# Kernel optimization log

Hardware: AMD Instinct MI355X
Metric: run time of the kernel (lower is better)

The kernel has to match this reference:

```python
import jax, jax.numpy as jnp
import numpy as np

N = 30000        # nodes
E = 600000       # edges
R = 32           # relations
NB = 30          # num_bases
D = 128          # entity_dim == hidden_dim == output_dim
H = 8            # heads, head dim C = D // H = 16
NUM_ENT = 100000
NGRAPH = 16      # graphs in batch
L = 2            # num_rgcn_layers == num_transformer_layers
EPS = 1e-5


def _ln(x, g, b):
    mu = x.mean(-1, keepdims=True)
    var = ((x - mu) ** 2).mean(-1, keepdims=True)
    return (x - mu) * jax.lax.rsqrt(var + EPS) * g + b


def setup_inputs() -> dict:
    key = jax.random.key(0)
    ks = iter(jax.random.split(key, 48))

    def nrm(shape, s=0.05):
        return jax.random.normal(next(ks), shape, jnp.float32) * s

    inp = {}
    inp["node_ids"] = jax.random.randint(next(ks), (N,), 0, NUM_ENT)
    inp["edge_index"] = jax.random.randint(next(ks), (2, E), 0, N)
    inp["edge_type"] = jax.random.randint(next(ks), (E,), 0, R)
    inp["batch"] = jnp.sort(jax.random.randint(next(ks), (N,), 0, NGRAPH))
    inp["entity_emb"] = nrm((NUM_ENT, D)).at[0].set(0.0)  # padding_idx=0
    inp["rel_emb"] = nrm((R, D)).at[0].set(0.0)           # padding_idx=0
    inp["rgcn_comp"] = nrm((L, R, NB))
    inp["rgcn_bases"] = nrm((L, NB, D, D))
    inp["rgcn_root"] = nrm((L, D, D))
    inp["rgcn_bias"] = jnp.zeros((L, D), jnp.float32)
    inp["rgcn_ln_g"] = jnp.ones((L, D), jnp.float32)
    inp["rgcn_ln_b"] = jnp.zeros((L, D), jnp.float32)
    inp["tr_wq"] = nrm((L, D, D)); inp["tr_bq"] = jnp.zeros((L, D), jnp.float32)
    inp["tr_wk"] = nrm((L, D, D)); inp["tr_bk"] = jnp.zeros((L, D), jnp.float32)
    inp["tr_wv"] = nrm((L, D, D)); inp["tr_bv"] = jnp.zeros((L, D), jnp.float32)
    inp["tr_we"] = nrm((L, D, D))                          # lin_edge (bias=False in PyG)
    inp["tr_wskip"] = nrm((L, D, D)); inp["tr_bskip"] = jnp.zeros((L, D), jnp.float32)
    inp["tr_ln_g"] = jnp.ones((L, D), jnp.float32)
    inp["tr_ln_b"] = jnp.zeros((L, D), jnp.float32)
    return inp


def reference(node_ids, edge_index, edge_type, batch, entity_emb, rel_emb,
              rgcn_comp, rgcn_bases, rgcn_root, rgcn_bias, rgcn_ln_g, rgcn_ln_b,
              tr_wq, tr_bq, tr_wk, tr_bk, tr_wv, tr_bv, tr_we, tr_wskip, tr_bskip,
              tr_ln_g, tr_ln_b):
    src, tgt = edge_index[0], edge_index[1]
    C = D // H
    x = entity_emb[node_ids]            # [N, D]
    edge_attr = rel_emb[edge_type]      # [E, D]

    # ---- RGCN layers: basis decomposition, mean aggregation per (target, relation) ----
    seg = tgt * R + edge_type
    cnt = jax.ops.segment_sum(jnp.ones((E,), jnp.float32), seg, num_segments=N * R)
    inv = jnp.where(cnt > 0, 1.0 / jnp.maximum(cnt, 1.0), 0.0)   # [N*R]
    for l in range(L):
        agg = jax.ops.segment_sum(x[src], seg, num_segments=N * R)   # [N*R, D]
        agg = (agg * inv[:, None]).reshape(N, R, D)
        w = jnp.einsum('rb,bio->rio', rgcn_comp[l], rgcn_bases[l])   # [R, D, D]
        x = jnp.einsum('nri,rio->no', agg, w) + x @ rgcn_root[l] + rgcn_bias[l]
        x = jax.nn.relu(_ln(x, rgcn_ln_g[l], rgcn_ln_b[l]))          # dropout = identity (eval)

    # ---- TransformerConv layers: edge-conditioned multi-head attention ----
    for l in range(L):
        q = (x @ tr_wq[l] + tr_bq[l]).reshape(N, H, C)
        k = (x @ tr_wk[l] + tr_bk[l]).reshape(N, H, C)
        v = (x @ tr_wv[l] + tr_bv[l]).reshape(N, H, C)
        e = (edge_attr @ tr_we[l]).reshape(E, H, C)
        kj = k[src] + e                                              # [E, H, C]
        vj = v[src] + e
        alpha = jnp.einsum('ehc,ehc->eh', q[tgt], kj) / np.float32(np.sqrt(C))
        m = jax.ops.segment_max(alpha, tgt, num_segments=N)          # [N, H]
        a = jnp.exp(alpha - m[tgt])
        denom = jax.ops.segment_sum(a, tgt, num_segments=N)
        a = a / jnp.maximum(denom[tgt], 1e-16)                       # softmax per target node
        out = jax.ops.segment_sum((vj * a[:, :, None]).reshape(E, D), tgt, num_segments=N)
        out = out + x @ tr_wskip[l] + tr_bskip[l]                    # root/skip connection
        out = jax.nn.relu(_ln(out, tr_ln_g[l], tr_ln_b[l]))          # dropout = identity (eval)
        x = x + out                                                  # dims match -> residual

    cnt_g = jax.ops.segment_sum(jnp.ones((N,), jnp.float32), batch, num_segments=NGRAPH)
    graph_emb = jax.ops.segment_sum(x, batch, num_segments=NGRAPH) / jnp.maximum(cnt_g, 1.0)[:, None]
    return x, graph_emb
```

## Files before the change

kernel.cpp:

```cpp
#include <hip/hip_runtime.h>

#define NN 30000
#define NE 600000
#define RR 32
#define NBASE 30
#define NG 16

typedef long long i64;
typedef unsigned short ushort;
typedef short bf16x8 __attribute__((ext_vector_type(8)));
typedef float f32x4 __attribute__((ext_vector_type(4)));

__device__ __forceinline__ ushort f2bf(float f){
  unsigned u = __float_as_uint(f);
  u += 0x7fffu + ((u >> 16) & 1u);
  return (ushort)(u >> 16);
}
__device__ __forceinline__ float bf2f(ushort u){
  return __uint_as_float(((unsigned)u) << 16);
}
__device__ __forceinline__ unsigned pk2(float a, float b){
  return (unsigned)f2bf(a) | ((unsigned)f2bf(b) << 16);
}

__global__ void k_gather(const float* __restrict__ emb, const int* __restrict__ ids,
                         float* __restrict__ x, ushort* __restrict__ xb){
  int t = blockIdx.x*256 + threadIdx.x;
  if (t >= NN*32) return;
  int n = t >> 5, c = t & 31;
  float4 v = ((const float4*)emb)[(i64)ids[n]*32 + c];
  ((float4*)x)[(i64)n*32 + c] = v;
  *(uint2*)&xb[(i64)n*128 + c*4] = make_uint2(pk2(v.x, v.y), pk2(v.z, v.w));
}

__global__ void k_cnt(const int* __restrict__ tgt, const int* __restrict__ ety,
                      float* __restrict__ cnt){
  int e = blockIdx.x*256 + threadIdx.x;
  if (e >= NE) return;
  atomicAdd(&cnt[(i64)tgt[e]*RR + ety[e]], 1.0f);
}

__global__ void k_hist_blk(const int* __restrict__ ety, int* __restrict__ hist){
  __shared__ int lh[RR];
  if (threadIdx.x < RR) lh[threadIdx.x] = 0;
  __syncthreads();
  int e0 = blockIdx.x*2048 + threadIdx.x;
  #pragma unroll
  for (int i = 0; i < 8; i++){
    int e = e0 + i*256;
    if (e < NE) atomicAdd(&lh[ety[e]], 1);
  }
  __syncthreads();
  if (threadIdx.x < RR){
    int v = lh[threadIdx.x];
    if (v) atomicAdd(&hist[threadIdx.x], v);
  }
}

__global__ void k_scan(const int* __restrict__ hist, int* __restrict__ base,
                       int* __restrict__ cursor, int* __restrict__ pb,
                       int* __restrict__ pb64){
  if (threadIdx.x != 0 || blockIdx.x != 0) return;
  int s = 0, p = 0, p64 = 0;
  for (int r = 0; r < RR; r++){
    base[r] = s; cursor[r] = s; pb[r] = p; pb64[r] = p64;
    s += hist[r]; p += (hist[r] + 127) >> 7; p64 += (hist[r] + 63) >> 6;
  }
  base[RR] = s; pb[RR] = p; pb64[RR] = p64;
}

__global__ __launch_bounds__(256) void k_scatter_blk(const int* __restrict__ ety,
    int* __restrict__ cursor, int* __restrict__ eord){
  __shared__ int lh[RR];
  __shared__ int lb[RR];
  if (threadIdx.x < RR) lh[threadIdx.x] = 0;
  __syncthreads();
  int e0 = blockIdx.x*2048 + threadIdx.x;
  #pragma unroll
  for (int i = 0; i < 8; i++){
    int e = e0 + i*256;
    if (e < NE) atomicAdd(&lh[ety[e]], 1);
  }
  __syncthreads();
  if (threadIdx.x < RR){
    int c = lh[threadIdx.x];
    lb[threadIdx.x] = c ? atomicAdd(&cursor[threadIdx.x], c) : 0;
  }
  __syncthreads();
  if (threadIdx.x < RR) lh[threadIdx.x] = 0;
  __syncthreads();
  #pragma unroll
  for (int i = 0; i < 8; i++){
    int e = e0 + i*256;
    if (e < NE){
      int r = ety[e];
      int loc = atomicAdd(&lh[r], 1);
      eord[lb[r] + loc] = e;
    }
  }
}

__global__ void k_hist2(const int* __restrict__ etgt, int* __restrict__ hist2){
  int e = blockIdx.x*256 + threadIdx.x;
  if (e >= NE) return;
  atomicAdd(&hist2[etgt[e]], 1);
}

__global__ __launch_bounds__(1024) void k_scan2(const int* __restrict__ hist2,
    int* __restrict__ rowptr, int* __restrict__ cursor2){
  __shared__ int s[1024];
  int t = threadIdx.x;
  int base = t*30;
  int loc[30];
  int sum = 0;
  #pragma unroll
  for (int i = 0; i < 30; i++){
    int v = (base+i < NN) ? hist2[base+i] : 0;
    loc[i] = sum; sum += v;
  }
  s[t] = sum; __syncthreads();
  for (int off = 1; off < 1024; off <<= 1){
    int v = (t >= off) ? s[t-off] : 0;
    __syncthreads();
    s[t] += v;
    __syncthreads();
  }
  int excl = (t > 0) ? s[t-1] : 0;
  #pragma unroll
  for (int i = 0; i < 30; i++){
    int idx = base + i;
    if (idx <= NN){
      rowptr[idx] = excl + loc[i];
      if (idx < NN) cursor2[idx] = excl + loc[i];
    }
  }
}

__global__ void k_scatter2(const int* __restrict__ etgt, const int* __restrict__ esrc,
                           const int* __restrict__ ety, int* __restrict__ cursor2,
                           int2* __restrict__ se2, int* __restrict__ pos2){
  int e = blockIdx.x*256 + threadIdx.x;
  if (e >= NE) return;
  int q = atomicAdd(&cursor2[etgt[e]], 1);
  se2[q] = make_int2(esrc[e], ety[e]);
  pos2[e] = q;
}

__global__ void k_basis(const float* __restrict__ comp, const float* __restrict__ bases,
                        float* __restrict__ wT, ushort* __restrict__ wTb){
  int t = blockIdx.x*256 + threadIdx.x;
  int r = t >> 14, rem = t & 16383, c = rem >> 7, kk = rem & 127;
  float acc = 0.f;
  for (int b = 0; b < NBASE; b++)
    acc += comp[r*NBASE + b] * bases[(i64)b*16384 + kk*128 + c];
  wT[t] = acc;
  wTb[t] = f2bf(acc);
}

__global__ void k_tw(const float* __restrict__ root, const float* __restrict__ wq,
                     const float* __restrict__ wk, const float* __restrict__ wv,
                     const float* __restrict__ wsk, ushort* __restrict__ out){
  int z = blockIdx.y;
  const float* srcs[5] = {root, wq, wk, wv, wsk};
  const float* S = srcs[z >> 1] + (i64)(z & 1)*16384;
  int idx = blockIdx.x*256 + threadIdx.x;
  int c = idx >> 7, kk = idx & 127;
  out[(i64)z*16384 + idx] = f2bf(S[kk*128 + c]);
}


__global__ __launch_bounds__(256, 2) void k_mm_mfma(const ushort* __restrict__ xb,
    const ushort* __restrict__ wTb, const float* __restrict__ bias,
    float* __restrict__ Y, int nrows){
  __shared__ ushort Xs[16384];
  __shared__ ushort Ws[16384];
  int t = threadIdx.x;
  int row0 = blockIdx.x * 128;
  for (int i = t; i < 2048; i += 256){
    int row = i >> 4, c = i & 15;
    *(uint4*)((char*)Ws + row*256 + ((c*16) ^ ((row&7)<<4))) =
        *(const uint4*)((const char*)wTb + row*256 + c*16);
    int gr = min(row0 + row, nrows - 1);
    *(uint4*)((char*)Xs + row*256 + ((c*16) ^ ((row&7)<<4))) =
        *(const uint4*)((const char*)(xb + (i64)gr*128) + c*16);
  }
  __syncthreads();
  int w = t >> 6, l = t & 63;
  int wm = w >> 1, wn = w & 1;
  int lrow = l & 15, lg = l >> 4;
  int swz = (lrow & 7) << 4;
  const char* pX = (const char*)Xs + (wm*64 + lrow)*256;
  const char* pW = (const char*)Ws + (wn*64 + lrow)*256;
  f32x4 acc[4][4] = {};
  #pragma unroll
  for (int ks = 0; ks < 4; ks++){
    int kb = (16*lg + 64*ks) ^ swz;
    bf16x8 a[4], bx[4];
    #pragma unroll
    for (int ns = 0; ns < 4; ns++) a[ns]  = *(const bf16x8*)(pW + ns*4096 + kb);
    #pragma unroll
    for (int ms = 0; ms < 4; ms++) bx[ms] = *(const bf16x8*)(pX + ms*4096 + kb);
    #pragma unroll
    for (int ms = 0; ms < 4; ms++)
      #pragma unroll
      for (int ns = 0; ns < 4; ns++)
        acc[ms][ns] = __builtin_amdgcn_mfma_f32_16x16x32_bf16(a[ns], bx[ms], acc[ms][ns], 0, 0, 0);
  }
  #pragma unroll
  for (int ms = 0; ms < 4; ms++){
    int m = row0 + wm*64 + ms*16 + lrow;
    if (m >= nrows) continue;
    #pragma unroll
    for (int ns = 0; ns < 4; ns++){
      int n0 = wn*64 + ns*16 + 4*lg;
      float4 bv = *(const float4*)&bias[n0];
      f32x4 v = acc[ms][ns];
      *(float4*)&Y[(i64)m*128 + n0] =
          make_float4(v[0]+bv.x, v[1]+bv.y, v[2]+bv.z, v[3]+bv.w);
    }
  }
}

__global__ __launch_bounds__(256, 2) void k_mm4(const ushort* __restrict__ xb,
    const ushort* __restrict__ wTb, int layer,
    const float* __restrict__ biq, const float* __restrict__ bik,
    const float* __restrict__ biv, const float* __restrict__ bisk,
    ushort* __restrict__ qo, ushort* __restrict__ ko, ushort* __restrict__ vo,
    float* __restrict__ z, int nrows){
  __shared__ ushort Xs[16384];
  __shared__ ushort Ws[16384];
  int t = threadIdx.x;
  int row0 = blockIdx.x * 128;
  for (int i = t; i < 2048; i += 256){
    int row = i >> 4, c = i & 15;
    int gr = min(row0 + row, nrows - 1);
    *(uint4*)((char*)Xs + row*256 + ((c*16) ^ ((row&7)<<4))) =
        *(const uint4*)((const char*)(xb + (i64)gr*128) + c*16);
  }
  int w = t >> 6, l = t & 63;
  int wm = w >> 1, wn = w & 1;
  int lrow = l & 15, lg = l >> 4;
  int swz = (lrow & 7) << 4;
  const char* pX = (const char*)Xs + (wm*64 + lrow)*256;
  const char* pW = (const char*)Ws + (wn*64 + lrow)*256;
  const float* biases[4] = {biq, bik, biv, bisk};
  ushort* outs[3] = {qo, ko, vo};
  #pragma unroll 1
  for (int arr = 0; arr < 4; arr++){
    const ushort* Wg = wTb + (i64)(2 + 2*arr + layer)*16384;
    __syncthreads();
    for (int i = t; i < 2048; i += 256){
      int row = i >> 4, c = i & 15;
      *(uint4*)((char*)Ws + row*256 + ((c*16) ^ ((row&7)<<4))) =
          *(const uint4*)((const char*)Wg + row*256 + c*16);
    }
    __syncthreads();
    f32x4 acc[4][4] = {};
    #pragma unroll
    for (int ks = 0; ks < 4; ks++){
      int kb = (16*lg + 64*ks) ^ swz;
      bf16x8 a[4], bx[4];
      #pragma unroll
      for (int ns = 0; ns < 4; ns++) a[ns]  = *(const bf16x8*)(pW + ns*4096 + kb);
      #pragma unroll
      for (int ms = 0; ms < 4; ms++) bx[ms] = *(const bf16x8*)(pX + ms*4096 + kb);
      #pragma unroll
      for (int ms = 0; ms < 4; ms++)
        #pragma unroll
        for (int ns = 0; ns < 4; ns++)
          acc[ms][ns] = __builtin_amdgcn_mfma_f32_16x16x32_bf16(a[ns], bx[ms], acc[ms][ns], 0, 0, 0);
    }
    const float* bias = biases[arr];
    #pragma unroll
    for (int ms = 0; ms < 4; ms++){
      int m = row0 + wm*64 + ms*16 + lrow;
      if (m >= nrows) continue;
      #pragma unroll
      for (int ns = 0; ns < 4; ns++){
        int n0 = wn*64 + ns*16 + 4*lg;
        float4 bv = *(const float4*)&bias[n0];
        f32x4 v = acc[ms][ns];
        if (arr < 3){
          *(uint2*)&outs[arr][(i64)m*128 + n0] =
              make_uint2(pk2(v[0]+bv.x, v[1]+bv.y), pk2(v[2]+bv.z, v[3]+bv.w));
        } else {
          *(float4*)&z[(i64)m*128 + n0] =
              make_float4(v[0]+bv.x, v[1]+bv.y, v[2]+bv.z, v[3]+bv.w);
        }
      }
    }
  }
}

__global__ __launch_bounds__(256, 2) void k_edge_mfma(const int* __restrict__ esrc,
    const int* __restrict__ etgt, const int* __restrict__ eord,
    const int* __restrict__ pos2, const int* __restrict__ hist,
    const int* __restrict__ base, const int* __restrict__ pb,
    const float* __restrict__ cnt, const ushort* __restrict__ xb,
    const ushort* __restrict__ wb, ushort* __restrict__ y){
  __shared__ ushort Xs[16384];
  __shared__ ushort Ws[16384];
  __shared__ int s_src[128];
  __shared__ int s_p2[128];
  __shared__ float s_inv[128];
  int b = blockIdx.x;
  int r = -1;
  #pragma unroll 1
  for (int i = 0; i < RR; i++){
    if (b >= pb[i] && b < pb[i+1]) { r = i; break; }
  }
  if (r < 0) return;
  int chunk = b - pb[r];
  int rowbase = base[r] + chunk*128;
  int nvalid = min(128, hist[r] - chunk*128);
  int t = threadIdx.x;
  if (t < 128){
    bool valid = t < nvalid;
    int eid = eord[rowbase + (valid ? t : 0)];
    s_src[t] = esrc[eid];
    s_p2[t]  = valid ? pos2[eid] : NE;
    s_inv[t] = valid ? (1.0f / cnt[(i64)etgt[eid]*RR + r]) : 0.0f;
  }
  __syncthreads();
  const ushort* Wg = wb + (i64)r*16384;
  for (int i = t; i < 2048; i += 256){
    int row = i >> 4, c = i & 15;
    *(uint4*)((char*)Ws + row*256 + ((c*16) ^ ((row&7)<<4))) =
        *(const uint4*)((const char*)Wg + row*256 + c*16);
    *(uint4*)((char*)Xs + row*256 + ((c*16) ^ ((row&7)<<4))) =
        *(const uint4*)((const char*)(xb + (i64)s_src[row]*128) + c*16);
  }
  __syncthreads();
  int w = t >> 6, l = t & 63;
  int wm = w >> 1, wn = w & 1;
  int lrow = l & 15, lg = l >> 4;
  int swz = (lrow & 7) << 4;
  const char* pX = (const char*)Xs + (wm*64 + lrow)*256;
  const char* pW = (const char*)Ws + (wn*64 + lrow)*256;
  f32x4 acc[4][4] = {};
  #pragma unroll
  for (int ks = 0; ks < 4; ks++){
    int kb = (16*lg + 64*ks) ^ swz;
    bf16x8 a[4], bx[4];
    #pragma unroll
    for (int ns = 0; ns < 4; ns++) a[ns]  = *(const bf16x8*)(pW + ns*4096 + kb);
    #pragma unroll
    for (int ms = 0; ms < 4; ms++) bx[ms] = *(const bf16x8*)(pX + ms*4096 + kb);
    #pragma unroll
    for (int ms = 0; ms < 4; ms++)
      #pragma unroll
      for (int ns = 0; ns < 4; ns++)
        acc[ms][ns] = __builtin_amdgcn_mfma_f32_16x16x32_bf16(a[ns], bx[ms], acc[ms][ns], 0, 0, 0);
  }
  #pragma unroll
  for (int ms = 0; ms < 4; ms++){
    int m = wm*64 + ms*16 + lrow;
    float sc = s_inv[m];
    i64 yrow = (i64)s_p2[m] * 128;
    #pragma unroll
    for (int ns = 0; ns < 4; ns++){
      int n0 = wn*64 + ns*16 + 4*lg;
      f32x4 v = acc[ms][ns];
      *(uint2*)&y[yrow + n0] = make_uint2(pk2(v[0]*sc, v[1]*sc), pk2(v[2]*sc, v[3]*sc));
    }
  }
}

__global__ __launch_bounds__(256) void k_edge_atomic(const int* __restrict__ esrc,
    const int* __restrict__ etgt, const int* __restrict__ eord,
    const int* __restrict__ hist, const int* __restrict__ base,
    const int* __restrict__ pb, const float* __restrict__ cnt,
    const float* __restrict__ x, const float* __restrict__ wT,
    float* __restrict__ z){
  __shared__ float Xs[64][132];
  __shared__ int s_src[64];
  __shared__ int s_tgt[64];
  __shared__ float s_inv[64];
  int b = blockIdx.x;
  int r = -1;
  #pragma unroll 1
  for (int i = 0; i < RR; i++){
    if (b >= pb[i] && b < pb[i+1]) { r = i; break; }
  }
  if (r < 0) return;
  int chunk = b - pb[r];
  int rowbase = base[r] + chunk*64;
  int cnt_r = hist[r];
  if (threadIdx.x < 64){
    int i = threadIdx.x;
    bool valid = (chunk*64 + i) < cnt_r;
    int eid = valid ? eord[rowbase + i] : 0;
    int sv = valid ? esrc[eid] : 0;
    int tv = valid ? etgt[eid] : 0;
    s_src[i] = sv; s_tgt[i] = tv;
    s_inv[i] = valid ? (1.0f / cnt[(i64)tv*RR + r]) : 0.0f;
  }
  __syncthreads();
  for (int idx = threadIdx.x; idx < 64*32; idx += 256){
    int rr = idx >> 5, c4 = idx & 31;
    *(float4*)&Xs[rr][c4*4] = ((const float4*)x)[(i64)s_src[rr]*32 + c4];
  }
  __syncthreads();
  const float* W = wT + (i64)r*16384;
  int m = threadIdx.x & 15, cg = threadIdx.x >> 4;
  float acc[4][8] = {};
  #pragma unroll 2
  for (int k4 = 0; k4 < 128; k4 += 4){
    float4 xv[4], wv[8];
    #pragma unroll
    for (int i = 0; i < 4; i++) xv[i] = *(float4*)&Xs[m + 16*i][k4];
    #pragma unroll
    for (int j = 0; j < 8; j++) wv[j] = *(const float4*)&W[(i64)(cg + 16*j)*128 + k4];
    #pragma unroll
    for (int i = 0; i < 4; i++)
      #pragma unroll
      for (int j = 0; j < 8; j++)
        acc[i][j] += xv[i].x*wv[j].x + xv[i].y*wv[j].y + xv[i].z*wv[j].z + xv[i].w*wv[j].w;
  }
  #pragma unroll
  for (int i = 0; i < 4; i++){
    int rr = m + 16*i;
    float sc = s_inv[rr];
    i64 o = (i64)s_tgt[rr]*128;
    #pragma unroll
    for (int j = 0; j < 8; j++)
      atomicAdd(&z[o + cg + 16*j], acc[i][j]*sc);
  }
}

__global__ void k_seg(const int* __restrict__ rowptr, const ushort* __restrict__ y,
                      const float* __restrict__ z, const float* __restrict__ g,
                      const float* __restrict__ b, float* __restrict__ x,
                      ushort* __restrict__ xb){
  int t = (blockIdx.x*256 + threadIdx.x) >> 6;
  int l = threadIdx.x & 63;
  if (t >= NN) return;
  int q0 = rowptr[t], q1 = rowptr[t+1];
  float ax = 0.f, ay = 0.f;
  for (int q = q0; q < q1; q++){
    ushort2 u = *(const ushort2*)&y[(i64)q*128 + 2*l];
    ax += bf2f(u.x); ay += bf2f(u.y);
  }
  float2 zv = *(const float2*)&z[(i64)t*128 + 2*l];
  float tx = ax + zv.x, ty = ay + zv.y;
  float s = tx + ty;
  #pragma unroll
  for (int o = 1; o < 64; o <<= 1) s += __shfl_xor(s, o);
  float mu = s * 0.0078125f;
  float dx = tx - mu, dy = ty - mu;
  float s2 = dx*dx + dy*dy;
  #pragma unroll
  for (int o = 1; o < 64; o <<= 1) s2 += __shfl_xor(s2, o);
  float rs = rsqrtf(s2 * 0.0078125f + 1e-5f);
  float2 gg = *(const float2*)&g[2*l];
  float2 bb = *(const float2*)&b[2*l];
  float o0 = fmaxf(dx*rs*gg.x + bb.x, 0.f);
  float o1 = fmaxf(dy*rs*gg.y + bb.y, 0.f);
  *(float2*)&x[(i64)t*128 + 2*l] = make_float2(o0, o1);
  xb[(i64)t*128 + 2*l]     = f2bf(o0);
  xb[(i64)t*128 + 2*l + 1] = f2bf(o1);
}

__global__ void k_lnrelu(const float* __restrict__ z, const float* __restrict__ g,
                         const float* __restrict__ b, float* __restrict__ xo,
                         ushort* __restrict__ xb){
  int w = (blockIdx.x*256 + threadIdx.x) >> 6;
  int l = threadIdx.x & 63;
  if (w >= NN) return;
  float2 v = *(const float2*)&z[(i64)w*128 + 2*l];
  float s = v.x + v.y;
  #pragma unroll
  for (int o = 1; o < 64; o <<= 1) s += __shfl_xor(s, o);
  float mu = s * 0.0078125f;
  float dx = v.x - mu, dy = v.y - mu;
  float s2 = dx*dx + dy*dy;
  #pragma unroll
  for (int o = 1; o < 64; o <<= 1) s2 += __shfl_xor(s2, o);
  float rs = rsqrtf(s2 * 0.0078125f + 1e-5f);
  float2 gg = *(const float2*)&g[2*l];
  float2 bb = *(const float2*)&b[2*l];
  float o0 = fmaxf(dx*rs*gg.x + bb.x, 0.f);
  float o1 = fmaxf(dy*rs*gg.y + bb.y, 0.f);
  *(float2*)&xo[(i64)w*128 + 2*l] = make_float2(o0, o1);
  xb[(i64)w*128 + 2*l]     = f2bf(o0);
  xb[(i64)w*128 + 2*l + 1] = f2bf(o1);
}

__global__ void k_ew(const float* __restrict__ rel, const float* __restrict__ we,
                     float* __restrict__ ew){
  int t = blockIdx.x*256 + threadIdx.x;
  int r = t >> 7, c = t & 127;
  float acc = 0.f;
  for (int k = 0; k < 128; k++) acc += rel[r*128 + k] * we[k*128 + c];
  ew[t] = acc;
}

__global__ __launch_bounds__(256) void k_attn(const int2* __restrict__ se2,
    const int* __restrict__ rowptr,
    const ushort* __restrict__ qbb, const ushort* __restrict__ kbb,
    const ushort* __restrict__ vbb, const float* __restrict__ ew,
    const float* __restrict__ sk, const float* __restrict__ g,
    const float* __restrict__ b, float* __restrict__ x, ushort* __restrict__ xb){
  __shared__ float sew[RR*128];
  for (int i = threadIdx.x; i < RR*32; i += 256)
    ((float4*)sew)[i] = ((const float4*)ew)[i];
  __syncthreads();
  int t = (blockIdx.x*256 + threadIdx.x) >> 6;
  int l = threadIdx.x & 63;
  if (t >= NN) return;
  int q0 = rowptr[t], q1 = rowptr[t+1];
  unsigned qu = *(const unsigned*)&qbb[(i64)t*128 + 2*l];
  float qx = bf2f((ushort)qu), qy = bf2f((ushort)(qu >> 16));
  float m = -3.0e38f, den = 0.f, ox = 0.f, oy = 0.f;
  if (q0 < q1){
    int2 sr = se2[q0];
    unsigned ku = *(const unsigned*)&kbb[(i64)sr.x*128 + 2*l];
    unsigned vu = *(const unsigned*)&vbb[(i64)sr.x*128 + 2*l];
    int r = sr.y;
    for (int q = q0; q < q1; q++){
      unsigned kun = 0, vun = 0; int rn = 0;
      if (q + 1 < q1){
        int2 srn = se2[q+1];
        kun = *(const unsigned*)&kbb[(i64)srn.x*128 + 2*l];
        vun = *(const unsigned*)&vbb[(i64)srn.x*128 + 2*l];
        rn = srn.y;
      }
      float2 ev = *(const float2*)&sew[r*128 + 2*l];
      float kx = bf2f((ushort)ku) + ev.x, ky = bf2f((ushort)(ku >> 16)) + ev.y;
      float p = qx*kx + qy*ky;
      p += __shfl_xor(p, 1); p += __shfl_xor(p, 2); p += __shfl_xor(p, 4);
      p *= 0.25f;
      float mn = fmaxf(m, p);
      float scl = __expf(m - mn);
      float wgt = __expf(p - mn);
      den = den*scl + wgt;
      ox = ox*scl + wgt*(bf2f((ushort)vu) + ev.x);
      oy = oy*scl + wgt*(bf2f((ushort)(vu >> 16)) + ev.y);
      m = mn;
      ku = kun; vu = vun; r = rn;
    }
  }
  float dn = fmaxf(den, 1e-16f);
  float2 zv = *(const float2*)&sk[(i64)t*128 + 2*l];
  float tx = ox/dn + zv.x, ty = oy/dn + zv.y;
  float s = tx + ty;
  #pragma unroll
  for (int o = 1; o < 64; o <<= 1) s += __shfl_xor(s, o);
  float mu = s * 0.0078125f;
  float dx = tx - mu, dy = ty - mu;
  float s2 = dx*dx + dy*dy;
  #pragma unroll
  for (int o = 1; o < 64; o <<= 1) s2 += __shfl_xor(s2, o);
  float rs = rsqrtf(s2 * 0.0078125f + 1e-5f);
  float2 gg = *(const float2*)&g[2*l];
  float2 bb = *(const float2*)&b[2*l];
  float o0 = fmaxf(dx*rs*gg.x + bb.x, 0.f);
  float o1 = fmaxf(dy*rs*gg.y + bb.y, 0.f);
  float2 xv = *(const float2*)&x[(i64)t*128 + 2*l];
  float nx = xv.x + o0, ny = xv.y + o1;
  *(float2*)&x[(i64)t*128 + 2*l] = make_float2(nx, ny);
  xb[(i64)t*128 + 2*l]     = f2bf(nx);
  xb[(i64)t*128 + 2*l + 1] = f2bf(ny);
}

__global__ void k_copy(const float* __restrict__ x, float* __restrict__ out){
  int t = blockIdx.x*256 + threadIdx.x;
  if (t >= NN*32) return;
  ((float4*)out)[t] = ((const float4*)x)[t];
}

__global__ void k_cntg(const int* __restrict__ batch, float* __restrict__ cntg){
  __shared__ int lh[NG];
  if (threadIdx.x < NG) lh[threadIdx.x] = 0;
  __syncthreads();
  int n = blockIdx.x*256 + threadIdx.x;
  if (n < NN) atomicAdd(&lh[batch[n]], 1);
  __syncthreads();
  if (threadIdx.x < NG){
    int v = lh[threadIdx.x];
    if (v) atomicAdd(&cntg[threadIdx.x], (float)v);
  }
}

__global__ void k_pool(const float* __restrict__ x, const int* __restrict__ batch,
                       float* __restrict__ gsum){
  __shared__ float acc[NG*128];
  for (int i = threadIdx.x; i < NG*128; i += 256) acc[i] = 0.f;
  __syncthreads();
  int per = (NN + gridDim.x - 1) / gridDim.x;
  int n0 = blockIdx.x*per, n1 = min(n0 + per, NN);
  int sub = threadIdx.x >> 5, c4 = threadIdx.x & 31;
  for (int n = n0 + sub; n < n1; n += 8){
    int g = batch[n];
    float4 xv = ((const float4*)x)[(i64)n*32 + c4];
    atomicAdd(&acc[g*128 + c4*4 + 0], xv.x);
    atomicAdd(&acc[g*128 + c4*4 + 1], xv.y);
    atomicAdd(&acc[g*128 + c4*4 + 2], xv.z);
    atomicAdd(&acc[g*128 + c4*4 + 3], xv.w);
  }
  __syncthreads();
  for (int i = threadIdx.x; i < NG*128; i += 256) atomicAdd(&gsum[i], acc[i]);
}

__global__ void k_poolfin(const float* __restrict__ gsum, const float* __restrict__ cntg,
                          float* __restrict__ gout){
  int t = blockIdx.x*256 + threadIdx.x;
  int g = t >> 7;
  gout[t] = gsum[t] / fmaxf(cntg[g], 1.0f);
}

extern "C" void kernel_launch(void* const* d_in, const int* in_sizes, int n_in,
                              void* d_out, int out_size, void* d_ws, size_t ws_size,
                              hipStream_t stream) {
  const int*   node_ids = (const int*)d_in[0];
  const int*   eidx  = (const int*)d_in[1];
  const int*   esrc  = eidx;
  const int*   etgt  = eidx + NE;
  const int*   ety   = (const int*)d_in[2];
  const int*   batch = (const int*)d_in[3];
  const float* ent   = (const float*)d_in[4];
  const float* rel   = (const float*)d_in[5];
  const float* comp  = (const float*)d_in[6];
  const float* bases = (const float*)d_in[7];
  const float* root  = (const float*)d_in[8];
  const float* rbias = (const float*)d_in[9];
  const float* rlng  = (const float*)d_in[10];
  const float* rlnb  = (const float*)d_in[11];
  const float* wq    = (const float*)d_in[12];
  const float* bq    = (const float*)d_in[13];
  const float* wk    = (const float*)d_in[14];
  const float* bk    = (const float*)d_in[15];
  const float* wv    = (const float*)d_in[16];
  const float* bv    = (const float*)d_in[17];
  const float* we    = (const float*)d_in[18];
  const float* wsk   = (const float*)d_in[19];
  const float* bsk   = (const float*)d_in[20];
  const float* tlng  = (const float*)d_in[21];
  const float* tlnb  = (const float*)d_in[22];
  float* out = (float*)d_out;

  char* wp = (char*)d_ws;
  auto alloc = [&](size_t bytes)->void*{
    void* p = (void*)wp;
    wp += (bytes + 255) & ~(size_t)255;
    return p;
  };
  float*    x     = (float*)alloc((size_t)NN*128*4);
  ushort*   xb    = (ushort*)alloc((size_t)NN*128*2);
  float*    z     = (float*)alloc((size_t)NN*128*4);
  ushort*   qbb   = (ushort*)alloc((size_t)NN*128*2);
  ushort*   kbb   = (ushort*)alloc((size_t)NN*128*2);
  ushort*   vbb   = (ushort*)alloc((size_t)NN*128*2);
  float*    cnt   = (float*)alloc((size_t)NN*RR*4);
  float*    wbT   = (float*)alloc((size_t)RR*16384*4);
  ushort*   wbTb  = (ushort*)alloc((size_t)RR*16384*2);
  ushort*   wTb   = (ushort*)alloc((size_t)10*16384*2);
  float*    ew    = (float*)alloc((size_t)RR*128*4);
  int*      eord  = (int*)alloc((size_t)NE*4);
  int*      pos2  = (int*)alloc((size_t)NE*4);
  int2*     se2   = (int2*)alloc((size_t)NE*8);
  int*      hist  = (int*)alloc(RR*4);
  int*      base  = (int*)alloc((RR+1)*4);
  int*      cursor= (int*)alloc(RR*4);
  int*      pb    = (int*)alloc((RR+1)*4);
  int*      pb64  = (int*)alloc((RR+1)*4);
  int*      hist2 = (int*)alloc((size_t)NN*4);
  int*      rowptr= (int*)alloc((size_t)(NN+1)*4);
  int*      cursor2=(int*)alloc((size_t)NN*4);
  float*    cntg  = (float*)alloc(NG*4);
  float*    gsum  = (float*)alloc((size_t)NG*128*4);
  size_t ybytes = (size_t)(NE + 8)*128*2;
  ushort*   y     = (ushort*)alloc(ybytes);
  bool fast = ((char*)y + ybytes) <= ((char*)d_ws + ws_size);

  dim3 B(256);

  hipMemsetAsync(cnt, 0, (size_t)NN*RR*4, stream);
  hipMemsetAsync(hist, 0, RR*4, stream);
  hipMemsetAsync(hist2, 0, (size_t)NN*4, stream);

  k_gather<<<3750, B, 0, stream>>>(ent, node_ids, x, xb);
  k_cnt<<<2344, B, 0, stream>>>(etgt, ety, cnt);
  k_hist_blk<<<294, B, 0, stream>>>(ety, hist);
  k_scan<<<1, 1, 0, stream>>>(hist, base, cursor, pb, pb64);
  k_scatter_blk<<<294, B, 0, stream>>>(ety, cursor, eord);
  k_hist2<<<2344, B, 0, stream>>>(etgt, hist2);
  k_scan2<<<1, 1024, 0, stream>>>(hist2, rowptr, cursor2);
  k_scatter2<<<2344, B, 0, stream>>>(etgt, esrc, ety, cursor2, se2, pos2);
  k_tw<<<dim3(64,10), B, 0, stream>>>(root, wq, wk, wv, wsk, wTb);

  for (int l = 0; l < 2; l++){
    k_basis<<<2048, B, 0, stream>>>(comp + l*RR*NBASE, bases + (i64)l*NBASE*16384, wbT, wbTb);
    k_mm_mfma<<<235, B, 0, stream>>>(xb, wTb + (i64)(0 + l)*16384, rbias + l*128, z, NN);
    if (fast){
      k_edge_mfma<<<4720, B, 0, stream>>>(esrc, etgt, eord, pos2, hist, base, pb, cnt, xb, wbTb, y);
      k_seg<<<7500, B, 0, stream>>>(rowptr, y, z, rlng + l*128, rlnb + l*128, x, xb);
    } else {
      k_edge_atomic<<<9407, B, 0, stream>>>(esrc, etgt, eord, hist, base, pb64, cnt, x, wbT, z);
      k_lnrelu<<<7500, B, 0, stream>>>(z, rlng + l*128, rlnb + l*128, x, xb);
    }
  }

  for (int l = 0; l < 2; l++){
    k_ew<<<16, B, 0, stream>>>(rel, we + (i64)l*16384, ew);
    k_mm4<<<235, B, 0, stream>>>(xb, wTb, l, bq + l*128, bk + l*128, bv + l*128,
                                 bsk + l*128, qbb, kbb, vbb, z, NN);
    k_attn<<<7500, B, 0, stream>>>(se2, rowptr, qbb, kbb, vbb, ew, z,
                                   tlng + l*128, tlnb + l*128, x, xb);
  }

  k_copy<<<3750, B, 0, stream>>>(x, out);
  hipMemsetAsync(gsum, 0, (size_t)NG*128*4, stream);
  hipMemsetAsync(cntg, 0, NG*4, stream);
  k_cntg<<<118, B, 0, stream>>>(batch, cntg);
  k_pool<<<120, B, 0, stream>>>(x, batch, gsum);
  k_poolfin<<<8, B, 0, stream>>>(gsum, cntg, out + (i64)NN*128);
}
```

Measured before the change: 949.9 us.

## Read MFMA weight fragments directly from global memory instead of LDS staging

In the three MFMA GEMM kernels (node matmul, fused q/k/v/skip matmul, per-relation edge matmul), the weight tile is no longer copied into shared memory. Each lane loads its bf16x8 weight fragments straight from global memory, which should mostly hit cache because all blocks share the same 32 KB weight. This halves LDS use per block, so launch bounds rise from 2 to 4 blocks per SM to increase occupancy, and k_mm4 drops the per-array barriers. The bf16 stores of x in the LN epilogues are also packed into one 32-bit write, at the cost of scattered global loads in the inner loop and tighter register limits.

New measurement: 963.7 us. Within noise of the previous version (+1.4%).

```diff
diff --git a/kernel.cpp b/kernel.cpp
--- a/kernel.cpp
+++ b/kernel.cpp
@@ -169,17 +169,14 @@
 }
 
 
-__global__ __launch_bounds__(256, 2) void k_mm_mfma(const ushort* __restrict__ xb,
+__global__ __launch_bounds__(256, 4) void k_mm_mfma(const ushort* __restrict__ xb,
     const ushort* __restrict__ wTb, const float* __restrict__ bias,
     float* __restrict__ Y, int nrows){
   __shared__ ushort Xs[16384];
-  __shared__ ushort Ws[16384];
   int t = threadIdx.x;
   int row0 = blockIdx.x * 128;
   for (int i = t; i < 2048; i += 256){
     int row = i >> 4, c = i & 15;
-    *(uint4*)((char*)Ws + row*256 + ((c*16) ^ ((row&7)<<4))) =
-        *(const uint4*)((const char*)wTb + row*256 + c*16);
     int gr = min(row0 + row, nrows - 1);
     *(uint4*)((char*)Xs + row*256 + ((c*16) ^ ((row&7)<<4))) =
         *(const uint4*)((const char*)(xb + (i64)gr*128) + c*16);
@@ -190,14 +187,14 @@
   int lrow = l & 15, lg = l >> 4;
   int swz = (lrow & 7) << 4;
   const char* pX = (const char*)Xs + (wm*64 + lrow)*256;
-  const char* pW = (const char*)Ws + (wn*64 + lrow)*256;
+  const char* pW = (const char*)wTb + (wn*64 + lrow)*256 + 16*lg;
   f32x4 acc[4][4] = {};
   #pragma unroll
   for (int ks = 0; ks < 4; ks++){
     int kb = (16*lg + 64*ks) ^ swz;
     bf16x8 a[4], bx[4];
     #pragma unroll
-    for (int ns = 0; ns < 4; ns++) a[ns]  = *(const bf16x8*)(pW + ns*4096 + kb);
+    for (int ns = 0; ns < 4; ns++) a[ns]  = *(const bf16x8*)(pW + ns*4096 + 64*ks);
     #pragma unroll
     for (int ms = 0; ms < 4; ms++) bx[ms] = *(const bf16x8*)(pX + ms*4096 + kb);
     #pragma unroll
@@ -221,14 +218,13 @@
   }
 }
 
-__global__ __launch_bounds__(256, 2) void k_mm4(const ushort* __restrict__ xb,
+__global__ __launch_bounds__(256, 4) void k_mm4(const ushort* __restrict__ xb,
     const ushort* __restrict__ wTb, int layer,
     const float* __restrict__ biq, const float* __restrict__ bik,
     const float* __restrict__ biv, const float* __restrict__ bisk,
     ushort* __restrict__ qo, ushort* __restrict__ ko, ushort* __restrict__ vo,
     float* __restrict__ z, int nrows){
   __shared__ ushort Xs[16384];
-  __shared__ ushort Ws[16384];
   int t = threadIdx.x;
   int row0 = blockIdx.x * 128;
   for (int i = t; i < 2048; i += 256){
@@ -237,31 +233,25 @@
     *(uint4*)((char*)Xs + row*256 + ((c*16) ^ ((row&7)<<4))) =
         *(const uint4*)((const char*)(xb + (i64)gr*128) + c*16);
   }
+  __syncthreads();
   int w = t >> 6, l = t & 63;
   int wm = w >> 1, wn = w & 1;
   int lrow = l & 15, lg = l >> 4;
   int swz = (lrow & 7) << 4;
   const char* pX = (const char*)Xs + (wm*64 + lrow)*256;
-  const char* pW = (const char*)Ws + (wn*64 + lrow)*256;
   const float* biases[4] = {biq, bik, biv, bisk};
   ushort* outs[3] = {qo, ko, vo};
   #pragma unroll 1
   for (int arr = 0; arr < 4; arr++){
-    const ushort* Wg = wTb + (i64)(2 + 2*arr + layer)*16384;
-    __syncthreads();
-    for (int i = t; i < 2048; i += 256){
-      int row = i >> 4, c = i & 15;
-      *(uint4*)((char*)Ws + row*256 + ((c*16) ^ ((row&7)<<4))) =
-          *(const uint4*)((const char*)Wg + row*256 + c*16);
-    }
-    __syncthreads();
+    const char* pW = (const char*)(wTb + (i64)(2 + 2*arr + layer)*16384)
+                     + (wn*64 + lrow)*256 + 16*lg;
     f32x4 acc[4][4] = {};
     #pragma unroll
     for (int ks = 0; ks < 4; ks++){
       int kb = (16*lg + 64*ks) ^ swz;
       bf16x8 a[4], bx[4];
       #pragma unroll
-      for (int ns = 0; ns < 4; ns++) a[ns]  = *(const bf16x8*)(pW + ns*4096 + kb);
+      for (int ns = 0; ns < 4; ns++) a[ns]  = *(const bf16x8*)(pW + ns*4096 + 64*ks);
       #pragma unroll
       for (int ms = 0; ms < 4; ms++) bx[ms] = *(const bf16x8*)(pX + ms*4096 + kb);
       #pragma unroll
@@ -292,14 +282,13 @@
   }
 }
 
-__global__ __launch_bounds__(256, 2) void k_edge_mfma(const int* __restrict__ esrc,
+__global__ __launch_bounds__(256, 4) void k_edge_mfma(const int* __restrict__ esrc,
     const int* __restrict__ etgt, const int* __restrict__ eord,
     const int* __restrict__ pos2, const int* __restrict__ hist,
     const int* __restrict__ base, const int* __restrict__ pb,
     const float* __restrict__ cnt, const ushort* __restrict__ xb,
     const ushort* __restrict__ wb, ushort* __restrict__ y){
   __shared__ ushort Xs[16384];
-  __shared__ ushort Ws[16384];
   __shared__ int s_src[128];
   __shared__ int s_p2[128];
   __shared__ float s_inv[128];
@@ -322,11 +311,8 @@
     s_inv[t] = valid ? (1.0f / cnt[(i64)etgt[eid]*RR + r]) : 0.0f;
   }
   __syncthreads();
-  const ushort* Wg = wb + (i64)r*16384;
   for (int i = t; i < 2048; i += 256){
     int row = i >> 4, c = i & 15;
-    *(uint4*)((char*)Ws + row*256 + ((c*16) ^ ((row&7)<<4))) =
-        *(const uint4*)((const char*)Wg + row*256 + c*16);
     *(uint4*)((char*)Xs + row*256 + ((c*16) ^ ((row&7)<<4))) =
         *(const uint4*)((const char*)(xb + (i64)s_src[row]*128) + c*16);
   }
@@ -336,14 +322,14 @@
   int lrow = l & 15, lg = l >> 4;
   int swz = (lrow & 7) << 4;
   const char* pX = (const char*)Xs + (wm*64 + lrow)*256;
-  const char* pW = (const char*)Ws + (wn*64 + lrow)*256;
+  const char* pW = (const char*)(wb + (i64)r*16384) + (wn*64 + lrow)*256 + 16*lg;
   f32x4 acc[4][4] = {};
   #pragma unroll
   for (int ks = 0; ks < 4; ks++){
     int kb = (16*lg + 64*ks) ^ swz;
     bf16x8 a[4], bx[4];
     #pragma unroll
-    for (int ns = 0; ns < 4; ns++) a[ns]  = *(const bf16x8*)(pW + ns*4096 + kb);
+    for (int ns = 0; ns < 4; ns++) a[ns]  = *(const bf16x8*)(pW + ns*4096 + 64*ks);
     #pragma unroll
     for (int ms = 0; ms < 4; ms++) bx[ms] = *(const bf16x8*)(pX + ms*4096 + kb);
     #pragma unroll
@@ -457,8 +443,7 @@
   float o0 = fmaxf(dx*rs*gg.x + bb.x, 0.f);
   float o1 = fmaxf(dy*rs*gg.y + bb.y, 0.f);
   *(float2*)&x[(i64)t*128 + 2*l] = make_float2(o0, o1);
-  xb[(i64)t*128 + 2*l]     = f2bf(o0);
-  xb[(i64)t*128 + 2*l + 1] = f2bf(o1);
+  *(unsigned*)&xb[(i64)t*128 + 2*l] = pk2(o0, o1);
 }
 
 __global__ void k_lnrelu(const float* __restrict__ z, const float* __restrict__ g,
@@ -482,8 +467,7 @@
   float o0 = fmaxf(dx*rs*gg.x + bb.x, 0.f);
   float o1 = fmaxf(dy*rs*gg.y + bb.y, 0.f);
   *(float2*)&xo[(i64)w*128 + 2*l] = make_float2(o0, o1);
-  xb[(i64)w*128 + 2*l]     = f2bf(o0);
-  xb[(i64)w*128 + 2*l + 1] = f2bf(o1);
+  *(unsigned*)&xb[(i64)w*128 + 2*l] = pk2(o0, o1);
 }
 
 __global__ void k_ew(const float* __restrict__ rel, const float* __restrict__ we,
@@ -559,8 +543,7 @@
   float2 xv = *(const float2*)&x[(i64)t*128 + 2*l];
   float nx = xv.x + o0, ny = xv.y + o1;
   *(float2*)&x[(i64)t*128 + 2*l] = make_float2(nx, ny);
-  xb[(i64)t*128 + 2*l]     = f2bf(nx);
-  xb[(i64)t*128 + 2*l + 1] = f2bf(ny);
+  *(unsigned*)&xb[(i64)t*128 + 2*l] = pk2(nx, ny);
 }
 
 __global__ void k_copy(const float* __restrict__ x, float* __restrict__ out){
```
